# Optimization experiments

Hardware: AMD Instinct MI355X
Metric: run time of the kernel (lower is better)

## Reference

```python
import jax, jax.numpy as jnp
import numpy as np

B, P, N, DIM = 2, 2, 1024, 256
HEADS, DH = 8, 64
INNER = HEADS * DH
HW = 32
C = HW * HW  # conv channels = h1*h2 = 1024
LN_EPS = 1e-5
BN_EPS = 1e-5


def setup_inputs() -> dict:
    key = jax.random.key(0)
    ks = jax.random.split(key, 10)
    return {
        "x": jax.random.normal(ks[0], (B, P, N, DIM), jnp.float32),
        "ln_g": jnp.ones((DIM,), jnp.float32),
        "ln_b": jnp.zeros((DIM,), jnp.float32),
        "w_qkv": jax.random.normal(ks[1], (DIM, 3 * INNER), jnp.float32) * DIM ** -0.5,
        "w_conv1": jax.random.normal(ks[2], (C, 2), jnp.float32) * 0.7,
        "w_conv2": jax.random.normal(ks[3], (C, 2), jnp.float32) * 0.7,
        "w_1x1": jax.random.normal(ks[4], (C, C), jnp.float32) * C ** -0.5,
        "bn_g": jnp.ones((C,), jnp.float32),
        "bn_b": jnp.zeros((C,), jnp.float32),
        "bn_m": jax.random.normal(ks[5], (C,), jnp.float32) * 0.1,
        "bn_v": jax.random.uniform(ks[6], (C,), jnp.float32, minval=0.5, maxval=1.5),
        "w_out": jax.random.normal(ks[7], (INNER, DIM), jnp.float32) * INNER ** -0.5,
        "b_out": jnp.zeros((DIM,), jnp.float32),
    }


def _dw_conv_w(a, w):
    # depthwise (1,2) kernel, reflection pad right by 1 (pad value = col W-2)
    ap = jnp.concatenate([a, a[..., -2:-1]], axis=-1)
    return ap[..., :-1] * w[:, 0][None, :, None, None] + ap[..., 1:] * w[:, 1][None, :, None, None]


def _dw_conv_h(a, w):
    # depthwise (2,1) kernel, reflection pad bottom by 1 (pad value = row H-2)
    ap = jnp.concatenate([a, a[:, :, -2:-1, :]], axis=2)
    return ap[:, :, :-1, :] * w[:, 0][None, :, None, None] + ap[:, :, 1:, :] * w[:, 1][None, :, None, None]


def reference(x, ln_g, ln_b, w_qkv, w_conv1, w_conv2, w_1x1, bn_g, bn_b, bn_m, bn_v, w_out, b_out):
    b, p, n, dim = x.shape
    # LayerNorm
    mu = jnp.mean(x, axis=-1, keepdims=True)
    var = jnp.mean(jnp.square(x - mu), axis=-1, keepdims=True)
    xn = (x - mu) * jax.lax.rsqrt(var + LN_EPS) * ln_g + ln_b
    # QKV projection, split heads
    qkv = xn @ w_qkv  # (b,p,n,3*inner)
    q, k, v = jnp.split(qkv, 3, axis=-1)
    split_heads = lambda t: t.reshape(b, p, n, HEADS, DH).transpose(0, 1, 3, 2, 4)
    q, k, v = map(split_heads, (q, k, v))  # (b,p,h,n,d)
    dots = jnp.einsum('bphnd,bphmd->bphnm', q, k) * (DH ** -0.5)  # (b,p,h,n,n)
    # rearrange scores: n=(h1 w1), m=(h2 w2) -> channels (h1 h2), spatial (w1 w2)
    a = dots.reshape(b, p, HEADS, HW, HW, HW, HW)
    a = a.transpose(0, 1, 2, 3, 5, 4, 6).reshape(b * p * HEADS, C, HW, HW)
    a = _dw_conv_w(a, w_conv1)
    a = _dw_conv_h(a, w_conv2)
    # 1x1 conv (no bias) + BatchNorm (inference) + SiLU
    a = jnp.einsum('bchw,oc->bohw', a, w_1x1)
    inv = jax.lax.rsqrt(bn_v + BN_EPS)
    a = (a - bn_m[None, :, None, None]) * (inv * bn_g)[None, :, None, None] + bn_b[None, :, None, None]
    a = a * jax.nn.sigmoid(a)
    # rearrange back to (b,p,h,n,n)
    a = a.reshape(b, p, HEADS, HW, HW, HW, HW).transpose(0, 1, 2, 3, 5, 4, 6).reshape(b, p, HEADS, n, n)
    attn = jax.nn.softmax(a, axis=-1)
    out = jnp.einsum('bphnm,bphmd->bphnd', attn, v)
    out = out.transpose(0, 1, 3, 2, 4).reshape(b, p, n, INNER)
    return out @ w_out + b_out
```

## Files before the change

### kernel.cpp

```cpp
#include <hip/hip_runtime.h>
#include <hip/hip_fp16.h>


#define DEV __device__ __forceinline__

typedef __attribute__((ext_vector_type(8))) _Float16 f16x8;
typedef __attribute__((ext_vector_type(4))) float f32x4;
typedef __attribute__((ext_vector_type(8))) unsigned short u16x8;

DEV float h2f_bits(unsigned short u) { __half h; *reinterpret_cast<unsigned short*>(&h) = u; return __half2float(h); }
DEV unsigned short f2h_bits(float f) { __half h = __float2half(f); return *reinterpret_cast<unsigned short*>(&h); }

__global__ __launch_bounds__(256) void prep_kernel(
    const float* __restrict__ wqkv, const float* __restrict__ w1x1,
    const float* __restrict__ wout,
    __half* __restrict__ WQKVT, __half* __restrict__ W1X1H, __half* __restrict__ WOTT) {
  int i0 = blockIdx.x * 256 + threadIdx.x;
  int stride = gridDim.x * 256;
  for (int i = i0; i < 1536 * 256; i += stride) {
    int j = i >> 8, k = i & 255;
    WQKVT[i] = __float2half(wqkv[k * 1536 + j]);
  }
  for (int i = i0; i < 1024 * 1024; i += stride) {
    int o = i >> 10, p = i & 1023;
    int blk = p >> 5, r = p & 31, a = r >> 3, bb = r & 7;
    int h1 = (blk >> 2) * 4 + a, h2 = (blk & 3) * 8 + bb;
    W1X1H[i] = __float2half(w1x1[o * 1024 + h1 * 32 + h2]);
  }
  for (int i = i0; i < 256 * 512; i += stride) {
    int j = i >> 9, k = i & 511;
    WOTT[i] = __float2half(wout[k * 256 + j]);
  }
}

__global__ __launch_bounds__(256) void ln_kernel(const float* __restrict__ x,
    const float* __restrict__ g, const float* __restrict__ b, __half* __restrict__ XN) {
  int row = blockIdx.x;
  int tid = threadIdx.x, lane = tid & 63, wid = tid >> 6;
  float xv = x[(size_t)row * 256 + tid];
  float s = xv, q = xv * xv;
#pragma unroll
  for (int off = 32; off; off >>= 1) { s += __shfl_xor(s, off); q += __shfl_xor(q, off); }
  __shared__ float rs[4], rq[4];
  if (lane == 0) { rs[wid] = s; rq[wid] = q; }
  __syncthreads();
  s = rs[0] + rs[1] + rs[2] + rs[3];
  q = rq[0] + rq[1] + rq[2] + rq[3];
  float mu = s * (1.f / 256.f);
  float var = q * (1.f / 256.f) - mu * mu;
  float r = rsqrtf(var + 1e-5f);
  XN[(size_t)row * 256 + tid] = __float2half((xv - mu) * r * g[tid] + b[tid]);
}

template <int BM, int BN, int BK, int WGN, int FM, int FN, class Epi>
__global__ __launch_bounds__(256) void gemm_bt(
    const __half* __restrict__ A, long long aStride,
    const __half* __restrict__ B, long long bStride,
    int K, Epi epi) {
  constexpr int CPR = BK / 8;
  constexpr int NCA = (BM * BK) / (8 * 256);
  constexpr int NCB = (BN * BK) / (8 * 256);
  constexpr int KSUB = BK / 32;
  __shared__ __align__(16) __half smA[2][BM * BK];
  __shared__ __align__(16) __half smB[2][BN * BK];
  const int tid = threadIdx.x;
  const int lane = tid & 63, wid = tid >> 6;
  const int wr = wid / WGN, wc = wid % WGN;
  const int gx = gridDim.x, gxy = gridDim.x * gridDim.y;
  const int nwg = gxy * gridDim.z;
  const int b_lin = blockIdx.x + blockIdx.y * gx + blockIdx.z * gxy;
  const int logical = (b_lin & 7) * (nwg >> 3) + (b_lin >> 3);
  const int bx = logical % gx, by = (logical / gx) % gridDim.y, bz = logical / gxy;
  const int img = bz;
  const int row0 = bx * BM;
  const int col0 = by * BN;
  const __half* Ab = A + (size_t)((long long)img * aStride);
  const __half* Bb = B + (size_t)((long long)img * bStride);
  f32x4 acc[FM][FN] = {};
  const int lr = lane & 15;
  const int kq = lane >> 4;

  auto swz = [](int c, int r) -> int {
    return (CPR == 8) ? (c ^ (r & 7)) : (c ^ ((r >> 1) & 3));
  };

  const __half* pA[NCA]; int dA[NCA];
  const __half* pB[NCB]; int dB[NCB];
#pragma unroll
  for (int it = 0; it < NCA; ++it) {
    int e = it * 256 + tid, r = e / CPR, c = e % CPR;
    pA[it] = Ab + (size_t)(row0 + r) * K + swz(c, r) * 8;
    dA[it] = r * BK + c * 8;
  }
#pragma unroll
  for (int it = 0; it < NCB; ++it) {
    int e = it * 256 + tid, r = e / CPR, c = e % CPR;
    pB[it] = Bb + (size_t)(col0 + r) * K + swz(c, r) * 8;
    dB[it] = r * BK + c * 8;
  }

  auto stage = [&](int buf, int kt) {
#pragma unroll
    for (int it = 0; it < NCA; ++it)
      __builtin_amdgcn_global_load_lds(
          (const __attribute__((address_space(1))) unsigned int*)(pA[it] + kt),
          (__attribute__((address_space(3))) unsigned int*)(&smA[buf][dA[it]]),
          16, 0, 0);
#pragma unroll
    for (int it = 0; it < NCB; ++it)
      __builtin_amdgcn_global_load_lds(
          (const __attribute__((address_space(1))) unsigned int*)(pB[it] + kt),
          (__attribute__((address_space(3))) unsigned int*)(&smB[buf][dB[it]]),
          16, 0, 0);
  };

  const int NT = K / BK;
  stage(0, 0);
  __syncthreads();
  int cur = 0;
  for (int t = 0; t < NT; ++t) {
    if (t + 1 < NT) stage(cur ^ 1, (t + 1) * BK);
#pragma unroll
    for (int kk = 0; kk < KSUB; ++kk) {
      f16x8 av[FM], bv[FN];
#pragma unroll
      for (int i = 0; i < FM; ++i) {
        int row = wr * FM * 16 + i * 16 + lr;
        int ch = swz(kk * 4 + kq, lr);
        av[i] = *reinterpret_cast<const f16x8*>(&smA[cur][row * BK + ch * 8]);
      }
#pragma unroll
      for (int j = 0; j < FN; ++j) {
        int row = wc * FN * 16 + j * 16 + lr;
        int ch = swz(kk * 4 + kq, lr);
        bv[j] = *reinterpret_cast<const f16x8*>(&smB[cur][row * BK + ch * 8]);
      }
#pragma unroll
      for (int i = 0; i < FM; ++i)
#pragma unroll
        for (int j = 0; j < FN; ++j)
          acc[i][j] = __builtin_amdgcn_mfma_f32_16x16x32_f16(av[i], bv[j], acc[i][j], 0, 0, 0);
    }
    __syncthreads();
    cur ^= 1;
  }

  const int orow = row0 + wr * FM * 16 + (lane >> 4) * 4;
  const int ocol = col0 + wc * FN * 16 + lr;
#pragma unroll
  for (int i = 0; i < FM; ++i)
#pragma unroll
    for (int j = 0; j < FN; ++j)
#pragma unroll
      for (int q = 0; q < 4; ++q)
        epi.store(img, orow + i * 16 + q, ocol + j * 16, acc[i][j][q]);
}

struct EpiQKV {
  __half *Q, *K, *V;
  DEV void store(int, int t, int j, float v) const {
    int part = j >> 9, inner = j & 511;
    int h = inner >> 6, d = inner & 63;
    int bp = t >> 10, n = t & 1023;
    size_t img = (size_t)(bp * 8 + h);
    if (part == 0)       Q[(img * 1024 + n) * 64 + d] = __float2half(v * 0.125f);
    else if (part == 1)  K[(img * 1024 + n) * 64 + d] = __float2half(v);
    else                 V[(img * 64 + d) * 1024 + n] = __float2half(v);
  }
};
struct EpiOut {
  float* out; const float* bias;
  DEV void store(int, int t, int j, float v) const {
    out[(size_t)t * 256 + j] = v + bias[j];
  }
};

__global__ __launch_bounds__(512) void qkconv_kernel(
    const __half* __restrict__ Q, const __half* __restrict__ Km,
    const float* __restrict__ wc1, const float* __restrict__ wc2,
    __half* __restrict__ AC) {
  constexpr int NP = 132;
  __shared__ __align__(16) char LDS[77824];
  __half* smA = (__half*)LDS;
  __half* smB = (__half*)(LDS + 16384);
  __half* Dt  = (__half*)LDS;
  __half* T   = (__half*)(LDS + 67584);
  const int tid = threadIdx.x;
  const int lane = tid & 63, wid = tid >> 6;
  const int wr = wid >> 2, wc = wid & 3;
  const int gx = gridDim.x, gxy = gx * gridDim.y;
  const int nwg = gxy * gridDim.z;
  const int b_lin = blockIdx.x + blockIdx.y * gx + blockIdx.z * gxy;
  const int logical = (b_lin & 7) * (nwg >> 3) + (b_lin >> 3);
  const int bx = logical % gx, by = (logical / gx) % gridDim.y, bz = logical / gxy;
  const int img = bz, row0 = bx * 128, col0 = by * 256;
  const __half* Qi = Q + ((size_t)img << 16);
  const __half* Ki = Km + ((size_t)img << 16);

#pragma unroll
  for (int it = 0; it < 2; ++it) {
    int e = it * 512 + tid, r = e >> 3, c = e & 7, sc = c ^ (r & 7);
    __builtin_amdgcn_global_load_lds(
        (const __attribute__((address_space(1))) unsigned int*)(Qi + (size_t)(row0 + r) * 64 + sc * 8),
        (__attribute__((address_space(3))) unsigned int*)(smA + r * 64 + c * 8), 16, 0, 0);
  }
#pragma unroll
  for (int it = 0; it < 4; ++it) {
    int e = it * 512 + tid, r = e >> 3, c = e & 7, sc = c ^ (r & 7);
    __builtin_amdgcn_global_load_lds(
        (const __attribute__((address_space(1))) unsigned int*)(Ki + (size_t)(col0 + r) * 64 + sc * 8),
        (__attribute__((address_space(3))) unsigned int*)(smB + r * 64 + c * 8), 16, 0, 0);
  }
  __syncthreads();

  const int lr = lane & 15, kq = lane >> 4;
  f32x4 acc[4][4] = {};
#pragma unroll
  for (int kk = 0; kk < 2; ++kk) {
    const int ch = (kk * 4 + kq) ^ (lr & 7);
    f16x8 av[4], bv[4];
#pragma unroll
    for (int i = 0; i < 4; ++i)
      av[i] = *reinterpret_cast<const f16x8*>(&smA[(wr * 64 + i * 16 + lr) * 64 + ch * 8]);
#pragma unroll
    for (int j = 0; j < 4; ++j)
      bv[j] = *reinterpret_cast<const f16x8*>(&smB[(wc * 64 + j * 16 + lr) * 64 + ch * 8]);
#pragma unroll
    for (int i = 0; i < 4; ++i)
#pragma unroll
      for (int j = 0; j < 4; ++j)
        acc[i][j] = __builtin_amdgcn_mfma_f32_16x16x32_f16(av[i], bv[j], acc[i][j], 0, 0, 0);
  }
  __syncthreads();

#pragma unroll
  for (int i = 0; i < 4; ++i) {
    int n0 = wr * 64 + i * 16 + kq * 4;
#pragma unroll
    for (int j = 0; j < 4; ++j) {
      int m = wc * 64 + j * 16 + lr;
      ushort4 o4;
      o4.x = f2h_bits(acc[i][j][0]); o4.y = f2h_bits(acc[i][j][1]);
      o4.z = f2h_bits(acc[i][j][2]); o4.w = f2h_bits(acc[i][j][3]);
      *reinterpret_cast<ushort4*>(Dt + m * NP + n0) = o4;
    }
  }
  __syncthreads();

  const int w2i = tid >> 7;
  const int b_  = (tid >> 4) & 7;
  const int a_  = (tid >> 2) & 3;
  const int w1q = (tid & 3) * 8;
  const int cch = (bx * 4 + a_) * 32 + (by * 8 + b_);
  const float u0 = wc1[2 * cch], u1 = wc1[2 * cch + 1];
  const float v0 = wc2[2 * cch], v1 = wc2[2 * cch + 1];
  const int cblk = (bx * 4 + by) * 32;
  __half* ACi = AC + ((size_t)img << 20);
  const int w1o = (tid >> 2) & 31, ck = tid & 3;

  for (int pass = 0; pass < 8; ++pass) {
    const int w2 = pass * 4 + w2i;
    const int w2n = (w2 < 31) ? w2 + 1 : 30;
    const __half* r0 = Dt + (b_ * 32 + w2) * NP + a_ * 32 + w1q;
    const __half* r1 = Dt + (b_ * 32 + w2n) * NP + a_ * 32 + w1q;
    float X[9];
    {
      ushort4 x0a = *reinterpret_cast<const ushort4*>(r0);
      ushort4 x0b = *reinterpret_cast<const ushort4*>(r0 + 4);
      ushort4 x1a = *reinterpret_cast<const ushort4*>(r1);
      ushort4 x1b = *reinterpret_cast<const ushort4*>(r1 + 4);
      X[0] = u0 * h2f_bits(x0a.x) + u1 * h2f_bits(x1a.x);
      X[1] = u0 * h2f_bits(x0a.y) + u1 * h2f_bits(x1a.y);
      X[2] = u0 * h2f_bits(x0a.z) + u1 * h2f_bits(x1a.z);
      X[3] = u0 * h2f_bits(x0a.w) + u1 * h2f_bits(x1a.w);
      X[4] = u0 * h2f_bits(x0b.x) + u1 * h2f_bits(x1b.x);
      X[5] = u0 * h2f_bits(x0b.y) + u1 * h2f_bits(x1b.y);
      X[6] = u0 * h2f_bits(x0b.z) + u1 * h2f_bits(x1b.z);
      X[7] = u0 * h2f_bits(x0b.w) + u1 * h2f_bits(x1b.w);
      X[8] = u0 * __half2float(r0[8]) + u1 * __half2float(r1[8]);
    }
#pragma unroll
    for (int k = 0; k < 8; ++k) {
      float ov = (w1q + k < 31) ? (v0 * X[k] + v1 * X[k + 1])
                                : (v0 * X[7] + v1 * X[6]);
      T[(w2i * 32 + w1q + k) * 40 + a_ * 8 + b_] = __float2half(ov);
    }
    __syncthreads();
    {
      const int w2o = pass * 4 + (tid >> 7);
      u16x8 v = *reinterpret_cast<const u16x8*>(T + ((tid >> 7) * 32 + w1o) * 40 + ck * 8);
      *reinterpret_cast<u16x8*>(ACi + (size_t)(w1o * 32 + w2o) * 1024 + cblk + ck * 8) = v;
    }
    __syncthreads();
  }
}

__global__ __launch_bounds__(512, 4) void gemm1x1pv(
    const __half* __restrict__ A,
    const __half* __restrict__ B, long long bStride,
    const __half* __restrict__ Vt,
    int K,
    const float* __restrict__ g, const float* __restrict__ b,
    const float* __restrict__ m, const float* __restrict__ vv,
    __half* __restrict__ O) {
  __shared__ __align__(16) char LDSRAW[81920];
  __half* smA = (__half*)LDSRAW;
  __half* smB = (__half*)(LDSRAW + 32768);
  __half* Plds = (__half*)LDSRAW;
  __half* Vlds = (__half*)(LDSRAW + 65536);
  const int tid = threadIdx.x;
  const int lane = tid & 63, wid = tid >> 6;
  const int wr = wid >> 1, wc = wid & 1;
  const int gx = gridDim.x, gxy = gx * gridDim.y;
  const int nwg = gxy * gridDim.z;
  const int b_lin = blockIdx.x + blockIdx.y * gx + blockIdx.z * gxy;
  const int logical = (b_lin & 7) * (nwg >> 3) + (b_lin >> 3);
  const int bx = logical % gx, by = (logical / gx) % gridDim.y, bz = logical / gxy;
  const int img = bz, row0 = bx * 256, col0 = by * 128;
  const __half* Ab = A;
  const __half* Bb = B + (size_t)((long long)img * bStride);
  const __half* Vti = Vt + ((size_t)img << 16);

  const __half* pA[2]; int dA[2];
#pragma unroll
  for (int it = 0; it < 2; ++it) {
    int e = it * 512 + tid, r = e >> 2, c = e & 3, sc = c ^ ((r >> 1) & 3);
    pA[it] = Ab + (size_t)(row0 + r) * K + sc * 8;
    dA[it] = r * 32 + c * 8;
  }
  const __half* pB1; int dB1;
  {
    int r = tid >> 2, c = tid & 3, sc = c ^ ((r >> 1) & 3);
    pB1 = Bb + (size_t)(col0 + r) * K + sc * 8;
    dB1 = r * 32 + c * 8;
  }
  auto stage = [&](int buf, int kt) {
#pragma unroll
    for (int it = 0; it < 2; ++it)
      __builtin_amdgcn_global_load_lds(
          (const __attribute__((address_space(1))) unsigned int*)(pA[it] + kt),
          (__attribute__((address_space(3))) unsigned int*)(&smA[buf * 8192 + dA[it]]),
          16, 0, 0);
    __builtin_amdgcn_global_load_lds(
        (const __attribute__((address_space(1))) unsigned int*)(pB1 + kt),
        (__attribute__((address_space(3))) unsigned int*)(&smB[buf * 4096 + dB1]),
        16, 0, 0);
  };
  auto stageV = [&](int ph) {
#pragma unroll
    for (int it = 0; it < 2; ++it) {
      int c = it * 512 + tid;
      int d = c >> 4, col8 = c & 15;
      __builtin_amdgcn_global_load_lds(
          (const __attribute__((address_space(1))) unsigned int*)(Vti + (size_t)d * 1024 + ph * 128 + ((col8 ^ (d & 7)) * 8)),
          (__attribute__((address_space(3))) unsigned int*)(Vlds + c * 8),
          16, 0, 0);
    }
  };

  const int lr = lane & 15, kq = lane >> 4;
  const int ch = kq ^ ((lr >> 1) & 3);
  const int aOff = (wr * 64 + lr) * 32 + ch * 8;
  const int bOff = (wc * 64 + lr) * 32 + ch * 8;
  f32x4 acc[4][4] = {};

  const int NT = K / 32;
  stage(0, 0);
  __syncthreads();
  int cur = 0;
  for (int t = 0; t < NT; ++t) {
    if (t + 1 < NT) stage(cur ^ 1, (t + 1) * 32);
    f16x8 av[4], bv[4];
#pragma unroll
    for (int i = 0; i < 4; ++i)
      av[i] = *reinterpret_cast<const f16x8*>(&smA[cur * 8192 + aOff + i * 512]);
#pragma unroll
    for (int j = 0; j < 4; ++j)
      bv[j] = *reinterpret_cast<const f16x8*>(&smB[cur * 4096 + bOff + j * 512]);
    __builtin_amdgcn_s_setprio(1);
#pragma unroll
    for (int i = 0; i < 4; ++i)
#pragma unroll
      for (int j = 0; j < 4; ++j)
        acc[i][j] = __builtin_amdgcn_mfma_f32_16x16x32_f16(av[i], bv[j], acc[i][j], 0, 0, 0);
    __builtin_amdgcn_s_setprio(0);
    __syncthreads();
    cur ^= 1;
  }
  stageV(0);
  const int ob = row0 + wr * 64;
#pragma unroll
  for (int ih = 0; ih < 2; ++ih) {
#pragma unroll
    for (int sh = 0; sh < 2; ++sh) {
      float v[2][2][4];
      float mx = -1e30f;
#pragma unroll
      for (int di = 0; di < 2; ++di) {
        int i = ih * 2 + di;
#pragma unroll
        for (int q = 0; q < 4; ++q) {
          int o = ob + i * 16 + kq * 4 + q;
          float sc = rsqrtf(vv[o] + 1e-5f) * g[o];
          float mo = m[o], bo = b[o];
#pragma unroll
          for (int dj = 0; dj < 2; ++dj) {
            float t = (acc[i][sh * 2 + dj][q] - mo) * sc + bo;
            t = t / (1.f + __expf(-t));
            v[di][dj][q] = t;
            mx = fmaxf(mx, t);
          }
        }
      }
#pragma unroll
      for (int off = 32; off; off >>= 1) mx = fmaxf(mx, __shfl_xor(mx, off));
      float sm = 0.f;
#pragma unroll
      for (int di = 0; di < 2; ++di)
#pragma unroll
        for (int dj = 0; dj < 2; ++dj)
#pragma unroll
          for (int q = 0; q < 4; ++q) {
            float e = __expf(v[di][dj][q] - mx);
            v[di][dj][q] = e; sm += e;
          }
#pragma unroll
      for (int off = 32; off; off >>= 1) sm += __shfl_xor(sm, off);
      float inv = 1.f / sm;
      const int ri = (wr * 2 + ih) * 4 + wc * 2 + sh;
      const int sw = (ri & 7) << 3;
      __half* Prow = Plds + ri * 1024;
#pragma unroll
      for (int di = 0; di < 2; ++di)
#pragma unroll
        for (int q = 0; q < 4; ++q) {
          int mo_ = (di * 16 + kq * 4 + q) * 32;
#pragma unroll
          for (int dj = 0; dj < 2; ++dj) {
            int mm = mo_ + dj * 16 + lr;
            Prow[mm ^ sw] = __float2half(v[di][dj][q] * inv);
          }
        }
    }
  }
  __syncthreads();
  {
    const int rt = wid >> 2, dt = wid & 3;
    const int arow = rt * 16 + lr;
    const int asw = (arow & 7) << 3;
    const int d = dt * 16 + lr;
    const __half* Pr = Plds + arow * 1024;
    const __half* Vr = Vlds + d * 128;
    f32x4 acc2 = {};
    for (int ph = 0; ph < 8; ++ph) {
#pragma unroll
      for (int kk2 = 0; kk2 < 4; ++kk2) {
        int m0 = ph * 128 + kk2 * 32 + kq * 8;
        f16x8 a = *reinterpret_cast<const f16x8*>(&Pr[m0 ^ asw]);
        f16x8 bb = *reinterpret_cast<const f16x8*>(&Vr[((kk2 * 4 + kq) ^ (d & 7)) * 8]);
        acc2 = __builtin_amdgcn_mfma_f32_16x16x32_f16(a, bb, acc2, 0, 0, 0);
      }
      if (ph < 7) {
        __syncthreads();
        stageV(ph + 1);
        __syncthreads();
      }
    }
#pragma unroll
    for (int q = 0; q < 4; ++q) {
      int ri = rt * 16 + kq * 4 + q;
      int n = (bx * 8 + (ri >> 2)) * 32 + by * 4 + (ri & 3);
      int dd = dt * 16 + lr;
      O[((size_t)((img >> 3) * 1024 + n)) * 512 + (img & 7) * 64 + dd] = __float2half(acc2[q]);
    }
  }
}

extern "C" void kernel_launch(void* const* d_in, const int* in_sizes, int n_in,
                              void* d_out, int out_size, void* d_ws, size_t ws_size,
                              hipStream_t stream) {
  const float* x     = (const float*)d_in[0];
  const float* ln_g  = (const float*)d_in[1];
  const float* ln_b  = (const float*)d_in[2];
  const float* w_qkv = (const float*)d_in[3];
  const float* wc1   = (const float*)d_in[4];
  const float* wc2   = (const float*)d_in[5];
  const float* w1x1  = (const float*)d_in[6];
  const float* bn_g  = (const float*)d_in[7];
  const float* bn_b  = (const float*)d_in[8];
  const float* bn_m  = (const float*)d_in[9];
  const float* bn_v  = (const float*)d_in[10];
  const float* w_out = (const float*)d_in[11];
  const float* b_out = (const float*)d_in[12];
  float* out = (float*)d_out;

  const size_t MB = 1024 * 1024;
  char* ws = (char*)d_ws;
  __half* ACb = (__half*)(ws + 64 * MB);
  char* p = ws + 128 * MB;
  __half* XN    = (__half*)p; p += 2 * MB;
  __half* WQKVT = (__half*)p; p += 1536 * 256 * 2;
  __half* W1X1H = (__half*)p; p += 2 * MB;
  __half* WOTT  = (__half*)p; p += 256 * 512 * 2;
  __half* Qb    = (__half*)p; p += 4 * MB;
  __half* Kb    = (__half*)p; p += 4 * MB;
  __half* Vtb   = (__half*)p; p += 4 * MB;
  __half* Ob    = (__half*)p; p += 4 * MB;

  prep_kernel<<<2048, 256, 0, stream>>>(w_qkv, w1x1, w_out, WQKVT, W1X1H, WOTT);
  ln_kernel<<<4096, 256, 0, stream>>>(x, ln_g, ln_b, XN);

  { EpiQKV e{Qb, Kb, Vtb};
    gemm_bt<128, 128, 64, 2, 4, 4, EpiQKV><<<dim3(32, 12, 1), 256, 0, stream>>>(
        XN, 0, WQKVT, 0, 256, e); }

  qkconv_kernel<<<dim3(8, 4, 32), 512, 0, stream>>>(Qb, Kb, wc1, wc2, ACb);

  gemm1x1pv<<<dim3(4, 8, 32), 512, 0, stream>>>(
      W1X1H, ACb, 1 << 20, Vtb, 1024, bn_g, bn_b, bn_m, bn_v, Ob);

  { EpiOut e{out, b_out};
    gemm_bt<64, 64, 64, 2, 2, 2, EpiOut><<<dim3(64, 4, 1), 256, 0, stream>>>(
        Ob, 0, WOTT, 0, 512, e); }
}
```

Before: 175.6 us.

## Coalesce weight transposes via LDS tiles and V transpose in QKV epilogue

Weight transpose-casts for w_qkv and w_out move out of the strided prep loop into a tiled LDS transpose kernel with vectorized loads and stores. The QKV GEMM becomes a dedicated kernel whose V-producing blocks stage the output tile in swizzled LDS and write transposed V with 16-byte stores, replacing scattered 2-byte stores. This targets uncoalesced global writes in the prep and QKV stages, at the cost of two extra launches and a larger specialized GEMM.

```diff
diff --git a/kernel.cpp b/kernel.cpp
--- a/kernel.cpp
+++ b/kernel.cpp
@@ -12,24 +12,39 @@
 DEV unsigned short f2h_bits(float f) { __half h = __float2half(f); return *reinterpret_cast<unsigned short*>(&h); }
 
 __global__ __launch_bounds__(256) void prep_kernel(
-    const float* __restrict__ wqkv, const float* __restrict__ w1x1,
-    const float* __restrict__ wout,
-    __half* __restrict__ WQKVT, __half* __restrict__ W1X1H, __half* __restrict__ WOTT) {
+    const float* __restrict__ w1x1, __half* __restrict__ W1X1H) {
   int i0 = blockIdx.x * 256 + threadIdx.x;
   int stride = gridDim.x * 256;
-  for (int i = i0; i < 1536 * 256; i += stride) {
-    int j = i >> 8, k = i & 255;
-    WQKVT[i] = __float2half(wqkv[k * 1536 + j]);
-  }
   for (int i = i0; i < 1024 * 1024; i += stride) {
     int o = i >> 10, p = i & 1023;
     int blk = p >> 5, r = p & 31, a = r >> 3, bb = r & 7;
     int h1 = (blk >> 2) * 4 + a, h2 = (blk & 3) * 8 + bb;
     W1X1H[i] = __float2half(w1x1[o * 1024 + h1 * 32 + h2]);
   }
-  for (int i = i0; i < 256 * 512; i += stride) {
-    int j = i >> 9, k = i & 511;
-    WOTT[i] = __float2half(wout[k * 256 + j]);
+}
+
+__global__ __launch_bounds__(256) void tcast_kernel(const float* __restrict__ src,
+    __half* __restrict__ dst, int R, int C) {
+  __shared__ __half T[64][80];
+  const int r0 = blockIdx.x * 64, c0 = blockIdx.y * 64;
+  {
+    int rr = threadIdx.x >> 2, cq = (threadIdx.x & 3) * 16;
+    const float4* s = reinterpret_cast<const float4*>(src + (size_t)(r0 + rr) * C + c0 + cq);
+#pragma unroll
+    for (int u = 0; u < 4; ++u) {
+      float4 f = s[u];
+      T[cq + u * 4 + 0][rr] = __float2half(f.x);
+      T[cq + u * 4 + 1][rr] = __float2half(f.y);
+      T[cq + u * 4 + 2][rr] = __float2half(f.z);
+      T[cq + u * 4 + 3][rr] = __float2half(f.w);
+    }
+  }
+  __syncthreads();
+  {
+    int cc = threadIdx.x >> 2, rq = (threadIdx.x & 3) * 16;
+    __half* d = dst + (size_t)(c0 + cc) * R + r0 + rq;
+    *reinterpret_cast<u16x8*>(d)     = *reinterpret_cast<const u16x8*>(&T[cc][rq]);
+    *reinterpret_cast<u16x8*>(d + 8) = *reinterpret_cast<const u16x8*>(&T[cc][rq + 8]);
   }
 }
 
@@ -51,6 +66,133 @@
   float r = rsqrtf(var + 1e-5f);
   XN[(size_t)row * 256 + tid] = __float2half((xv - mu) * r * g[tid] + b[tid]);
 }
+
+__global__ __launch_bounds__(256) void gemm_qkv(
+    const __half* __restrict__ A, const __half* __restrict__ B,
+    __half* __restrict__ Q, __half* __restrict__ Ko, __half* __restrict__ Vt) {
+  constexpr int BK = 64, K = 256;
+  __shared__ __align__(16) char RAW[65536];
+  __half* smA = (__half*)RAW;
+  __half* smB = (__half*)(RAW + 32768);
+  __half* Tld = (__half*)RAW;
+  const int tid = threadIdx.x;
+  const int lane = tid & 63, wid = tid >> 6;
+  const int wr = wid >> 1, wc = wid & 1;
+  const int gx = gridDim.x;
+  const int nwg = gx * gridDim.y;
+  const int b_lin = blockIdx.x + blockIdx.y * gx;
+  const int logical = (b_lin & 7) * (nwg >> 3) + (b_lin >> 3);
+  const int bx = logical % gx, by = logical / gx;
+  const int row0 = bx * 128, col0 = by * 128;
+  f32x4 acc[4][4] = {};
+  const int lr = lane & 15;
+  const int kq = lane >> 4;
+
+  const __half* pA[4]; int dA[4];
+  const __half* pB[4]; int dB[4];
+#pragma unroll
+  for (int it = 0; it < 4; ++it) {
+    int e = it * 256 + tid, r = e >> 3, c = e & 7, sc = c ^ (r & 7);
+    pA[it] = A + (size_t)(row0 + r) * K + sc * 8;
+    pB[it] = B + (size_t)(col0 + r) * K + sc * 8;
+    dA[it] = dB[it] = r * BK + c * 8;
+  }
+  auto stage = [&](int buf, int kt) {
+#pragma unroll
+    for (int it = 0; it < 4; ++it)
+      __builtin_amdgcn_global_load_lds(
+          (const __attribute__((address_space(1))) unsigned int*)(pA[it] + kt),
+          (__attribute__((address_space(3))) unsigned int*)(&smA[buf * 8192 + dA[it]]),
+          16, 0, 0);
+#pragma unroll
+    for (int it = 0; it < 4; ++it)
+      __builtin_amdgcn_global_load_lds(
+          (const __attribute__((address_space(1))) unsigned int*)(pB[it] + kt),
+          (__attribute__((address_space(3))) unsigned int*)(&smB[buf * 8192 + dB[it]]),
+          16, 0, 0);
+  };
+
+  const int NT = K / BK;
+  stage(0, 0);
+  __syncthreads();
+  int cur = 0;
+  for (int t = 0; t < NT; ++t) {
+    if (t + 1 < NT) stage(cur ^ 1, (t + 1) * BK);
+#pragma unroll
+    for (int kk = 0; kk < 2; ++kk) {
+      f16x8 av[4], bv[4];
+#pragma unroll
+      for (int i = 0; i < 4; ++i) {
+        int row = wr * 64 + i * 16 + lr;
+        int ch = (kk * 4 + kq) ^ (lr & 7);
+        av[i] = *reinterpret_cast<const f16x8*>(&smA[cur * 8192 + row * BK + ch * 8]);
+      }
+#pragma unroll
+      for (int j = 0; j < 4; ++j) {
+        int row = wc * 64 + j * 16 + lr;
+        int ch = (kk * 4 + kq) ^ (lr & 7);
+        bv[j] = *reinterpret_cast<const f16x8*>(&smB[cur * 8192 + row * BK + ch * 8]);
+      }
+#pragma unroll
+      for (int i = 0; i < 4; ++i)
+#pragma unroll
+        for (int j = 0; j < 4; ++j)
+          acc[i][j] = __builtin_amdgcn_mfma_f32_16x16x32_f16(av[i], bv[j], acc[i][j], 0, 0, 0);
+    }
+    __syncthreads();
+    cur ^= 1;
+  }
+
+  const int bp = row0 >> 10, n0 = row0 & 1023;
+  if (by < 8) {
+#pragma unroll
+    for (int i = 0; i < 4; ++i)
+#pragma unroll
+      for (int j = 0; j < 4; ++j)
+#pragma unroll
+        for (int q = 0; q < 4; ++q) {
+          int t = row0 + wr * 64 + i * 16 + kq * 4 + q;
+          int jj = col0 + wc * 64 + j * 16 + lr;
+          int part = jj >> 9, inner = jj & 511;
+          int h = inner >> 6, d = inner & 63;
+          int n = t & 1023;
+          size_t img = (size_t)((t >> 10) * 8 + h);
+          float v = acc[i][j][q];
+          if (part == 0) Q[(img * 1024 + n) * 64 + d] = __float2half(v * 0.125f);
+          else           Ko[(img * 1024 + n) * 64 + d] = __float2half(v);
+        }
+  } else {
+#pragma unroll
+    for (int i = 0; i < 4; ++i)
+#pragma unroll
+      for (int j = 0; j < 4; ++j)
+#pragma unroll
+        for (int q = 0; q < 4; ++q) {
+          int nl = wr * 64 + i * 16 + kq * 4 + q;
+          int jl = wc * 64 + j * 16 + lr;
+          int ch = (nl >> 3) ^ (jl & 7);
+          Tld[jl * 136 + ch * 8 + (nl & 7)] = __float2half(acc[i][j][q]);
+        }
+    __syncthreads();
+    const int jl = tid >> 1, hf = tid & 1;
+    const int d = jl & 63;
+    const int vimg = bp * 8 + (by - 8) * 2 + (jl >> 6);
+    __half* dst = Vt + ((size_t)(vimg * 64 + d)) * 1024 + n0 + hf * 64;
+#pragma unroll
+    for (int u = 0; u < 8; ++u) {
+      int cidx = (hf * 8 + u) ^ (jl & 7);
+      *reinterpret_cast<u16x8*>(dst + u * 8) =
+          *reinterpret_cast<const u16x8*>(Tld + jl * 136 + cidx * 8);
+    }
+  }
+}
+
+struct EpiOut {
+  float* out; const float* bias;
+  DEV void store(int, int t, int j, float v) const {
+    out[(size_t)t * 256 + j] = v + bias[j];
+  }
+};
 
 template <int BM, int BN, int BK, int WGN, int FM, int FN, class Epi>
 __global__ __launch_bounds__(256) void gemm_bt(
@@ -156,25 +298,6 @@
         epi.store(img, orow + i * 16 + q, ocol + j * 16, acc[i][j][q]);
 }
 
-struct EpiQKV {
-  __half *Q, *K, *V;
-  DEV void store(int, int t, int j, float v) const {
-    int part = j >> 9, inner = j & 511;
-    int h = inner >> 6, d = inner & 63;
-    int bp = t >> 10, n = t & 1023;
-    size_t img = (size_t)(bp * 8 + h);
-    if (part == 0)       Q[(img * 1024 + n) * 64 + d] = __float2half(v * 0.125f);
-    else if (part == 1)  K[(img * 1024 + n) * 64 + d] = __float2half(v);
-    else                 V[(img * 64 + d) * 1024 + n] = __float2half(v);
-  }
-};
-struct EpiOut {
-  float* out; const float* bias;
-  DEV void store(int, int t, int j, float v) const {
-    out[(size_t)t * 256 + j] = v + bias[j];
-  }
-};
-
 __global__ __launch_bounds__(512) void qkconv_kernel(
     const __half* __restrict__ Q, const __half* __restrict__ Km,
     const float* __restrict__ wc1, const float* __restrict__ wc2,
@@ -507,12 +630,12 @@
   __half* Vtb   = (__half*)p; p += 4 * MB;
   __half* Ob    = (__half*)p; p += 4 * MB;
 
-  prep_kernel<<<2048, 256, 0, stream>>>(w_qkv, w1x1, w_out, WQKVT, W1X1H, WOTT);
+  prep_kernel<<<1024, 256, 0, stream>>>(w1x1, W1X1H);
+  tcast_kernel<<<dim3(4, 24), 256, 0, stream>>>(w_qkv, WQKVT, 256, 1536);
+  tcast_kernel<<<dim3(8, 4), 256, 0, stream>>>(w_out, WOTT, 512, 256);
   ln_kernel<<<4096, 256, 0, stream>>>(x, ln_g, ln_b, XN);
 
-  { EpiQKV e{Qb, Kb, Vtb};
-    gemm_bt<128, 128, 64, 2, 4, 4, EpiQKV><<<dim3(32, 12, 1), 256, 0, stream>>>(
-        XN, 0, WQKVT, 0, 256, e); }
+  gemm_qkv<<<dim3(32, 12), 256, 0, stream>>>(XN, WQKVT, Qb, Kb, Vtb);
 
   qkconv_kernel<<<dim3(8, 4, 32), 512, 0, stream>>>(Qb, Kb, wc1, wc2, ACb);
 
```

Measured after the change: 169.0 us. -3.7%, faster.
